# Optimization experiments

Hardware: AMD Instinct MI355X
Metric: run time of the kernel (lower is better)

Reference implementation:

```python
import jax, jax.numpy as jnp
import numpy as np

D, NP, NC, ITERS = 2048, 64, 32, 3
B, L = 4, 4096
EPS = 1e-6


def setup_inputs() -> dict:
    key = jax.random.key(0)
    ks = jax.random.split(key, 10)
    sc = lambda k, shape, s: (jax.random.normal(k, shape, jnp.float32) * s)
    return {
        "x": jax.random.normal(ks[0], (B, L, D), jnp.float32),
        "prop_w": sc(ks[1], (NP, D), 0.02),
        "prop_b": jnp.zeros((NP,), jnp.float32),
        "constraint_mat": sc(ks[2], (NC, NP), 0.1),
        "polarity": sc(ks[3], (NC, NP), 0.1),
        "corr_w1": sc(ks[4], (2 * NP, 2 * NP), 0.08),
        "corr_b1": jnp.zeros((2 * NP,), jnp.float32),
        "corr_w2": sc(ks[5], (NP, 2 * NP), 0.08),
        "corr_b2": jnp.zeros((NP,), jnp.float32),
        "cons_w": sc(ks[6], (1, NC), 0.1),
        "cons_b": jnp.zeros((1,), jnp.float32),
        "emb_w": sc(ks[7], (D, NP), 0.02),
        "emb_b": jnp.zeros((D,), jnp.float32),
        "norm_w": jnp.ones((D,), jnp.float32),
    }


def reference(x, prop_w, prop_b, constraint_mat, polarity,
              corr_w1, corr_b1, corr_w2, corr_b2,
              cons_w, cons_b, emb_w, emb_b, norm_w):
    n_p = prop_w.shape[0]
    n_c = constraint_mat.shape[0]
    W = jax.nn.sigmoid(constraint_mat)  # [n_c, n_p] constraint strength
    P = jax.nn.sigmoid(polarity)        # [n_c, n_p] polarity

    def check(props):
        # mean_j(W_ij*p_j + P_ij*(1-p_j)) == (p @ W.T + (1-p) @ P.T) / n_p
        return (props @ W.T + (1.0 - props) @ P.T) / n_p  # [B,L,n_c]

    props = jax.nn.sigmoid(x @ prop_w.T + prop_b)  # [B,L,n_p]
    for _ in range(ITERS):
        violation = 1.0 - check(props)                 # [B,L,n_c]
        viol_signal = (violation @ W) / (n_c + 1e-06)  # [B,L,n_p]
        h = jnp.concatenate([props, viol_signal], axis=-1)  # [B,L,2*n_p]
        h = jax.nn.gelu(h @ corr_w1.T + corr_b1, approximate=False)
        props = jax.nn.sigmoid(h @ corr_w2.T + corr_b2)

    satisfaction = check(props)                              # [B,L,n_c]
    consistency = jax.nn.sigmoid(satisfaction @ cons_w.T + cons_b)  # [B,L,1]
    violation_loss = jnp.mean(1.0 - satisfaction)
    symbolic = props @ emb_w.T + emb_b                       # [B,L,D]
    y = x + symbolic * consistency
    y = y * jax.lax.rsqrt(jnp.mean(y * y, axis=-1, keepdims=True) + EPS) * norm_w
    return (y, props, satisfaction, consistency, violation_loss)
```

## Files before the change

kernel.cpp:

```cpp
#include <hip/hip_runtime.h>
#include <hip/hip_bf16.h>
#include <cstdint>

#define D     2048
#define NP    64
#define NC    32
#define T     16384

#define Y_OFF   0
#define P_OFF   33554432
#define S_OFF   34603008
#define C_OFF   35127296
#define L_OFF   35143680

#define WS_LPART 0
#define WS_SUMP  1024
#define WS_PWF   1056
#define WS_EF    66592
#define WS_W1F   132128
#define WS_W2F   140320
#define WS_WMF   144416
#define WS_WLF   145440

typedef short short8 __attribute__((ext_vector_type(8)));
typedef float f32x4 __attribute__((ext_vector_type(4)));

__device__ __forceinline__ float sigf(float z) { return 1.0f / (1.0f + __expf(-z)); }
__device__ __forceinline__ short f2bf(float f) {
  unsigned u = __float_as_uint(f);
  return (short)((u + 0x8000u) >> 16);
}
__device__ __forceinline__ unsigned pk2(float a, float b) {
  return ((unsigned)(unsigned short)f2bf(a)) | (((unsigned)(unsigned short)f2bf(b)) << 16);
}

__global__ __launch_bounds__(256) void k0_prep(const float* __restrict__ cm, const float* __restrict__ pol,
                                               const float* __restrict__ w1, const float* __restrict__ w2,
                                               const float* __restrict__ pw, const float* __restrict__ ew,
                                               float* __restrict__ ws) {
  int gid = blockIdx.x * 256 + threadIdx.x;
  int stride = gridDim.x * 256;
  short* pwF = (short*)(ws + WS_PWF);
  for (int idx = gid; idx < 64 * 4 * 64; idx += stride) {
    int kc = idx >> 8, jt = (idx >> 6) & 3, l = idx & 63;
    int j = 16 * jt + (l & 15), k = 32 * kc + 8 * (l >> 4);
    const float* src = &pw[(size_t)j * D + k];
    short8 v;
#pragma unroll
    for (int e = 0; e < 8; ++e) v[e] = f2bf(src[e]);
    *(short8*)&pwF[idx * 8] = v;
  }
  short* eF = (short*)(ws + WS_EF);
  for (int idx = gid; idx < 128 * 2 * 64; idx += stride) {
    int dt = idx >> 7, kc = (idx >> 6) & 1, l = idx & 63;
    int d = 16 * dt + (l & 15), j = 32 * kc + 8 * (l >> 4);
    const float* src = &ew[(size_t)d * NP + j];
    short8 v;
#pragma unroll
    for (int e = 0; e < 8; ++e) v[e] = f2bf(src[e]);
    *(short8*)&eF[idx * 8] = v;
  }
  short* w1F = (short*)(ws + WS_W1F);
  for (int idx = gid; idx < 8 * 4 * 64; idx += stride) {
    int nt = idx >> 8, kc = (idx >> 6) & 3, l = idx & 63;
    int m = 16 * nt + (l & 15), k = 32 * kc + 8 * (l >> 4);
    const float* src = &w1[(size_t)m * 128 + k];
    short8 v;
#pragma unroll
    for (int e = 0; e < 8; ++e) v[e] = f2bf(src[e]);
    *(short8*)&w1F[idx * 8] = v;
  }
  short* w2F = (short*)(ws + WS_W2F);
  for (int idx = gid; idx < 4 * 4 * 64; idx += stride) {
    int nt = idx >> 8, kc = (idx >> 6) & 3, l = idx & 63;
    int j = 16 * nt + (l & 15), k = 32 * kc + 8 * (l >> 4);
    const float* src = &w2[(size_t)j * 128 + k];
    short8 v;
#pragma unroll
    for (int e = 0; e < 8; ++e) v[e] = f2bf(src[e]);
    *(short8*)&w2F[idx * 8] = v;
  }
  short* wmF = (short*)(ws + WS_WMF);
  for (int idx = gid; idx < 2 * 2 * 64; idx += stride) {
    int nt = idx >> 7, kc = (idx >> 6) & 1, l = idx & 63;
    int i = 16 * nt + (l & 15), j = 32 * kc + 8 * (l >> 4);
    short8 v;
#pragma unroll
    for (int e = 0; e < 8; ++e)
      v[e] = f2bf(sigf(cm[i * 64 + j + e]) - sigf(pol[i * 64 + j + e]));
    *(short8*)&wmF[idx * 8] = v;
  }
  short* wlF = (short*)(ws + WS_WLF);
  for (int idx = gid; idx < 4 * 64; idx += stride) {
    int nt = idx >> 6, l = idx & 63;
    int j = 16 * nt + (l & 15), i0 = 8 * (l >> 4);
    short8 v;
#pragma unroll
    for (int e = 0; e < 8; ++e) v[e] = f2bf(sigf(cm[(i0 + e) * 64 + j]));
    *(short8*)&wlF[idx * 8] = v;
  }
  if (gid < NC) {
    float s = 0.f;
    for (int j = 0; j < NP; ++j) s += sigf(pol[gid * NP + j]);
    ws[WS_SUMP + gid] = s;
  }
}

__global__ __launch_bounds__(256) void k1_props(const float* __restrict__ x, const float* __restrict__ ws,
                                                const float* __restrict__ pb, float* __restrict__ props0) {
  __shared__ char XT[8192];
  int tid = threadIdx.x, lane = tid & 63;
  int jt = __builtin_amdgcn_readfirstlane(tid >> 6);
  int wv = tid >> 6;
  int t0 = blockIdx.x * 16;
  int lr = lane & 15, lg = lane >> 4;
  int c64 = tid & 63;
  const short* pwF = (const short*)(ws + WS_PWF);

  f32x4 acc = {0.f, 0.f, 0.f, 0.f};
  for (int c = 0; c < 8; ++c) {
    float4 st[4];
#pragma unroll
    for (int j = 0; j < 4; ++j)
      st[j] = *(const float4*)&x[(size_t)(t0 + wv + 4 * j) * D + 256 * c + 4 * c64];
    __syncthreads();
#pragma unroll
    for (int j = 0; j < 4; ++j) {
      int tt = wv + 4 * j;
      int off = (tt * 512 + 8 * c64) ^ ((tt & 7) << 4);
      *(uint2*)(XT + off) = make_uint2(pk2(st[j].x, st[j].y), pk2(st[j].z, st[j].w));
    }
    __syncthreads();
#pragma unroll
    for (int kcL = 0; kcL < 8; ++kcL) {
      const short8 b = *(const short8*)(XT + ((lr * 512 + 64 * kcL + 16 * lg) ^ ((lr & 7) << 4)));
      const short8 a = *(const short8*)&pwF[(((8 * c + kcL) * 4 + jt) * 64 + lane) * 8];
      acc = __builtin_amdgcn_mfma_f32_16x16x32_bf16(a, b, acc, 0, 0, 0);
    }
  }
  int j0 = 16 * jt + 4 * lg;
  const float4 pbv = *(const float4*)&pb[j0];
  float4 o;
  o.x = sigf(acc[0] + pbv.x); o.y = sigf(acc[1] + pbv.y);
  o.z = sigf(acc[2] + pbv.z); o.w = sigf(acc[3] + pbv.w);
  *(float4*)&props0[(size_t)(t0 + lr) * 64 + j0] = o;
}

__global__ __launch_bounds__(64) void k2_iter(const float* __restrict__ ws,
                                              const float* __restrict__ b1, const float* __restrict__ b2,
                                              const float* __restrict__ cw, const float* __restrict__ cb,
                                              const float* __restrict__ props0, float* __restrict__ out,
                                              float* __restrict__ lpart) {
  __shared__ char Lraw[9216];
  char* Hb = Lraw;
  char* H2b = Lraw + 4096;
  char* SBb = Lraw + 8192;
  int lane = threadIdx.x & 63;
  int lr = lane & 15, lg = lane >> 4;
  int t0 = blockIdx.x * 16;
  const short8* w1F = (const short8*)(ws + WS_W1F);
  const short8* w2F = (const short8*)(ws + WS_W2F);
  const short8* wmF = (const short8*)(ws + WS_WMF);
  const short8* wlF = (const short8*)(ws + WS_WLF);
  const float* SUMP = ws + WS_SUMP;

  float b1v[8], b2v[4], sumpv[2], cwv[2];
#pragma unroll
  for (int nt = 0; nt < 8; ++nt) b1v[nt] = b1[16 * nt + lr];
#pragma unroll
  for (int nt = 0; nt < 4; ++nt) b2v[nt] = b2[16 * nt + lr];
#pragma unroll
  for (int nt = 0; nt < 2; ++nt) { sumpv[nt] = SUMP[16 * nt + lr]; cwv[nt] = cw[16 * nt + lr]; }
  float cb0 = cb[0];

#pragma unroll
  for (int r = 0; r < 4; ++r) {
    int idx = r * 64 + lane;
    int t = idx >> 4, c4 = idx & 15;
    const float4 v = *(const float4*)&props0[(size_t)(t0 + t) * 64 + 4 * c4];
    int off = (t * 256 + c4 * 8) ^ ((t & 7) << 4);
    *(unsigned*)(Hb + off) = pk2(v.x, v.y);
    *(unsigned*)(Hb + off + 4) = pk2(v.z, v.w);
  }
  __syncthreads();

  const f32x4 zf = {0.f, 0.f, 0.f, 0.f};
  f32x4 s0, s1;

#define LDF(base, row, kelem, rowB) \
  (*(const short8*)((base) + ((((row) * (rowB)) + (kelem) * 2) ^ (((row) & 7) << 4))))
#define STBF(base, row, kelem, rowB, val) \
  (*(short*)((base) + ((((row) * (rowB)) + (kelem) * 2) ^ (((row) & 7) << 4))) = f2bf(val))

  for (int it = 0; it < 3; ++it) {
    short8 ap0 = LDF(Hb, lr, 8 * lg, 256);
    short8 ap1 = LDF(Hb, lr, 32 + 8 * lg, 256);
    s0 = zf; s1 = zf;
    s0 = __builtin_amdgcn_mfma_f32_16x16x32_bf16(ap0, wmF[0 * 64 + lane], s0, 0, 0, 0);
    s0 = __builtin_amdgcn_mfma_f32_16x16x32_bf16(ap1, wmF[1 * 64 + lane], s0, 0, 0, 0);
    s1 = __builtin_amdgcn_mfma_f32_16x16x32_bf16(ap0, wmF[2 * 64 + lane], s1, 0, 0, 0);
    s1 = __builtin_amdgcn_mfma_f32_16x16x32_bf16(ap1, wmF[3 * 64 + lane], s1, 0, 0, 0);
#pragma unroll
    for (int q = 0; q < 4; ++q) {
      int t = 4 * lg + q;
      STBF(SBb, t, lr, 64, 1.f - (s0[q] + sumpv[0]) * (1.f / 64.f));
      STBF(SBb, t, 16 + lr, 64, 1.f - (s1[q] + sumpv[1]) * (1.f / 64.f));
    }
    __syncthreads();

    short8 as = LDF(SBb, lr, 8 * lg, 64);
    f32x4 vv0 = __builtin_amdgcn_mfma_f32_16x16x32_bf16(as, wlF[0 * 64 + lane], zf, 0, 0, 0);
    f32x4 vv1 = __builtin_amdgcn_mfma_f32_16x16x32_bf16(as, wlF[1 * 64 + lane], zf, 0, 0, 0);
    f32x4 vv2 = __builtin_amdgcn_mfma_f32_16x16x32_bf16(as, wlF[2 * 64 + lane], zf, 0, 0, 0);
    f32x4 vv3 = __builtin_amdgcn_mfma_f32_16x16x32_bf16(as, wlF[3 * 64 + lane], zf, 0, 0, 0);
    const float vs = 1.0f / (32.0f + 1e-6f);
#pragma unroll
    for (int q = 0; q < 4; ++q) {
      int t = 4 * lg + q;
      STBF(Hb, t, 64 + lr, 256, vv0[q] * vs);
      STBF(Hb, t, 64 + 16 + lr, 256, vv1[q] * vs);
      STBF(Hb, t, 64 + 32 + lr, 256, vv2[q] * vs);
      STBF(Hb, t, 64 + 48 + lr, 256, vv3[q] * vs);
    }
    __syncthreads();

    short8 ah2 = LDF(Hb, lr, 64 + 8 * lg, 256);
    short8 ah3 = LDF(Hb, lr, 96 + 8 * lg, 256);
    f32x4 g1[8];
#pragma unroll
    for (int nt = 0; nt < 8; ++nt) {
      f32x4 a = zf;
      a = __builtin_amdgcn_mfma_f32_16x16x32_bf16(ap0, w1F[(nt * 4 + 0) * 64 + lane], a, 0, 0, 0);
      a = __builtin_amdgcn_mfma_f32_16x16x32_bf16(ap1, w1F[(nt * 4 + 1) * 64 + lane], a, 0, 0, 0);
      a = __builtin_amdgcn_mfma_f32_16x16x32_bf16(ah2, w1F[(nt * 4 + 2) * 64 + lane], a, 0, 0, 0);
      a = __builtin_amdgcn_mfma_f32_16x16x32_bf16(ah3, w1F[(nt * 4 + 3) * 64 + lane], a, 0, 0, 0);
      g1[nt] = a;
    }
#pragma unroll
    for (int nt = 0; nt < 8; ++nt) {
#pragma unroll
      for (int q = 0; q < 4; ++q) {
        float v = g1[nt][q] + b1v[nt];
        float gl = 0.5f * v * (1.0f + erff(v * 0.70710678118654752f));
        STBF(H2b, 4 * lg + q, 16 * nt + lr, 256, gl);
      }
    }
    __syncthreads();

    short8 ab0 = LDF(H2b, lr, 8 * lg, 256);
    short8 ab1 = LDF(H2b, lr, 32 + 8 * lg, 256);
    short8 ab2 = LDF(H2b, lr, 64 + 8 * lg, 256);
    short8 ab3 = LDF(H2b, lr, 96 + 8 * lg, 256);
#pragma unroll
    for (int nt = 0; nt < 4; ++nt) {
      f32x4 a = zf;
      a = __builtin_amdgcn_mfma_f32_16x16x32_bf16(ab0, w2F[(nt * 4 + 0) * 64 + lane], a, 0, 0, 0);
      a = __builtin_amdgcn_mfma_f32_16x16x32_bf16(ab1, w2F[(nt * 4 + 1) * 64 + lane], a, 0, 0, 0);
      a = __builtin_amdgcn_mfma_f32_16x16x32_bf16(ab2, w2F[(nt * 4 + 2) * 64 + lane], a, 0, 0, 0);
      a = __builtin_amdgcn_mfma_f32_16x16x32_bf16(ab3, w2F[(nt * 4 + 3) * 64 + lane], a, 0, 0, 0);
#pragma unroll
      for (int q = 0; q < 4; ++q) {
        int t = 4 * lg + q;
        float p = sigf(a[q] + b2v[nt]);
        STBF(Hb, t, 16 * nt + lr, 256, p);
        if (it == 2) out[P_OFF + (size_t)(t0 + t) * 64 + 16 * nt + lr] = p;
      }
    }
    __syncthreads();
  }

  {
    short8 ap0 = LDF(Hb, lr, 8 * lg, 256);
    short8 ap1 = LDF(Hb, lr, 32 + 8 * lg, 256);
    s0 = zf; s1 = zf;
    s0 = __builtin_amdgcn_mfma_f32_16x16x32_bf16(ap0, wmF[0 * 64 + lane], s0, 0, 0, 0);
    s0 = __builtin_amdgcn_mfma_f32_16x16x32_bf16(ap1, wmF[1 * 64 + lane], s0, 0, 0, 0);
    s1 = __builtin_amdgcn_mfma_f32_16x16x32_bf16(ap0, wmF[2 * 64 + lane], s1, 0, 0, 0);
    s1 = __builtin_amdgcn_mfma_f32_16x16x32_bf16(ap1, wmF[3 * 64 + lane], s1, 0, 0, 0);
    float ls = 0.f;
    float csum[4];
#pragma unroll
    for (int q = 0; q < 4; ++q) {
      int t = 4 * lg + q;
      float sa = (s0[q] + sumpv[0]) * (1.f / 64.f);
      float sb = (s1[q] + sumpv[1]) * (1.f / 64.f);
      out[S_OFF + (size_t)(t0 + t) * 32 + lr] = sa;
      out[S_OFF + (size_t)(t0 + t) * 32 + 16 + lr] = sb;
      ls += (1.f - sa) + (1.f - sb);
      csum[q] = cwv[0] * sa + cwv[1] * sb;
    }
#pragma unroll
    for (int m = 1; m <= 8; m <<= 1) {
#pragma unroll
      for (int q = 0; q < 4; ++q) csum[q] += __shfl_xor(csum[q], m);
    }
    if (lr == 0) {
#pragma unroll
      for (int q = 0; q < 4; ++q)
        out[C_OFF + t0 + 4 * lg + q] = sigf(csum[q] + cb0);
    }
#pragma unroll
    for (int m = 1; m <= 32; m <<= 1) ls += __shfl_xor(ls, m);
    if (lane == 0) lpart[blockIdx.x] = ls;
  }
#undef LDF
#undef STBF
}

__global__ __launch_bounds__(512, 4) void k3n(const float* __restrict__ x, const float* __restrict__ ws,
                                              const float* __restrict__ eb, const float* __restrict__ nw,
                                              const float* __restrict__ lpart, float* __restrict__ out) {
  __shared__ float ssp[8][16];
  __shared__ float sc16[16];
  int tid = threadIdx.x, lane = tid & 63;
  int wu = __builtin_amdgcn_readfirstlane(tid >> 6);
  int t0 = blockIdx.x * 16;
  int lr = lane & 15, lg = lane >> 4;
  const short* eF = (const short*)(ws + WS_EF);

  if (blockIdx.x == 0 && wu == 7) {
    float v = 0.f;
#pragma unroll
    for (int r = 0; r < 16; ++r) v += lpart[lane + 64 * r];
#pragma unroll
    for (int m = 1; m <= 32; m <<= 1) v += __shfl_xor(v, m);
    if (lane == 0) out[L_OFF] = v * (1.0f / (16384.0f * 32.0f));
  }

  const float* pr = out + P_OFF + (size_t)(t0 + lr) * 64 + 8 * lg;
  const float4 q0 = *(const float4*)pr;
  const float4 q1 = *(const float4*)(pr + 4);
  const float4 q2 = *(const float4*)(pr + 32);
  const float4 q3 = *(const float4*)(pr + 36);
  short8 p0, p1;
  p0[0] = f2bf(q0.x); p0[1] = f2bf(q0.y); p0[2] = f2bf(q0.z); p0[3] = f2bf(q0.w);
  p0[4] = f2bf(q1.x); p0[5] = f2bf(q1.y); p0[6] = f2bf(q1.z); p0[7] = f2bf(q1.w);
  p1[0] = f2bf(q2.x); p1[1] = f2bf(q2.y); p1[2] = f2bf(q2.z); p1[3] = f2bf(q2.w);
  p1[4] = f2bf(q3.x); p1[5] = f2bf(q3.y); p1[6] = f2bf(q3.z); p1[7] = f2bf(q3.w);

  float consv = out[C_OFF + t0 + lr];

  uint2 yv[16];
  float ss = 0.f;
#pragma unroll
  for (int dt2 = 0; dt2 < 16; ++dt2) {
    int dt = wu * 16 + dt2;
    const short8 e0 = *(const short8*)&eF[((dt * 2 + 0) * 64 + lane) * 8];
    const short8 e1 = *(const short8*)&eF[((dt * 2 + 1) * 64 + lane) * 8];
    f32x4 acc = {0.f, 0.f, 0.f, 0.f};
    acc = __builtin_amdgcn_mfma_f32_16x16x32_bf16(e0, p0, acc, 0, 0, 0);
    acc = __builtin_amdgcn_mfma_f32_16x16x32_bf16(e1, p1, acc, 0, 0, 0);
    int d0 = 16 * dt + 4 * lg;
    const float4 ebv = *(const float4*)&eb[d0];
    const float4 xv = *(const float4*)&x[(size_t)(t0 + lr) * D + d0];
    float y0 = fmaf(acc[0] + ebv.x, consv, xv.x);
    float y1 = fmaf(acc[1] + ebv.y, consv, xv.y);
    float y2 = fmaf(acc[2] + ebv.z, consv, xv.z);
    float y3 = fmaf(acc[3] + ebv.w, consv, xv.w);
    ss += y0 * y0 + y1 * y1 + y2 * y2 + y3 * y3;
    yv[dt2] = make_uint2(pk2(y0, y1), pk2(y2, y3));
  }
  ss += __shfl_xor(ss, 16);
  ss += __shfl_xor(ss, 32);
  if (lg == 0) ssp[wu][lr] = ss;
  __syncthreads();
  if (tid < 16) {
    float s = 0.f;
#pragma unroll
    for (int w = 0; w < 8; ++w) s += ssp[w][tid];
    sc16[tid] = rsqrtf(s * (1.0f / 2048.0f) + 1e-6f);
  }
  __syncthreads();
  float sc = sc16[lr];
#pragma unroll
  for (int dt2 = 0; dt2 < 16; ++dt2) {
    int d0 = 16 * (wu * 16 + dt2) + 4 * lg;
    const float4 nwv = *(const float4*)&nw[d0];
    uint2 p = yv[dt2];
    float4 o;
    o.x = __uint_as_float(p.x << 16) * sc * nwv.x;
    o.y = __uint_as_float(p.x & 0xffff0000u) * sc * nwv.y;
    o.z = __uint_as_float(p.y << 16) * sc * nwv.z;
    o.w = __uint_as_float(p.y & 0xffff0000u) * sc * nwv.w;
    *(float4*)&out[Y_OFF + (size_t)(t0 + lr) * D + d0] = o;
  }
}

extern "C" void kernel_launch(void* const* d_in, const int* in_sizes, int n_in,
                              void* d_out, int out_size, void* d_ws, size_t ws_size,
                              hipStream_t stream) {
  (void)in_sizes; (void)n_in; (void)out_size; (void)ws_size;
  const float* x   = (const float*)d_in[0];
  const float* pw  = (const float*)d_in[1];
  const float* pb  = (const float*)d_in[2];
  const float* cm  = (const float*)d_in[3];
  const float* pol = (const float*)d_in[4];
  const float* w1  = (const float*)d_in[5];
  const float* b1  = (const float*)d_in[6];
  const float* w2  = (const float*)d_in[7];
  const float* b2  = (const float*)d_in[8];
  const float* cw  = (const float*)d_in[9];
  const float* cb  = (const float*)d_in[10];
  const float* ew  = (const float*)d_in[11];
  const float* eb  = (const float*)d_in[12];
  const float* nw  = (const float*)d_in[13];
  float* out = (float*)d_out;
  float* ws  = (float*)d_ws;

  hipLaunchKernelGGL(k0_prep, dim3(128), dim3(256), 0, stream, cm, pol, w1, w2, pw, ew, ws);
  hipLaunchKernelGGL(k1_props, dim3(1024), dim3(256), 0, stream, x, ws, pb, out + Y_OFF);
  hipLaunchKernelGGL(k2_iter, dim3(1024), dim3(64), 0, stream, ws, b1, b2, cw, cb,
                     out + Y_OFF, out, ws + WS_LPART);
  hipLaunchKernelGGL(k3n, dim3(1024), dim3(512), 0, stream, x, ws, eb, nw,
                     ws + WS_LPART, out);
}
```

Baseline: 125.6 us.

## Fuse iterative correction kernel into embedding/RMSNorm kernel with single-wave prologue

Merges the per-token iteration kernel (k2) into the final embedding+norm kernel, so wave 0 of each 512-thread block runs the three correction iterations and the satisfaction/consistency step. Props and consistency then pass through LDS instead of global memory. The other waves prefetch their x rows into registers while wave 0 works, and wave 0 uses LDS waitcnt fences in place of block barriers. Initial props go to workspace instead of the y buffer, and the loss reduction moves to a tiny separate kernel. The trade-off is that seven waves idle during the serial iteration phase and the 16 float4 prefetch registers raise register pressure.

```diff
diff --git a/kernel.cpp b/kernel.cpp
--- a/kernel.cpp
+++ b/kernel.cpp
@@ -21,6 +21,7 @@
 #define WS_W2F   140320
 #define WS_WMF   144416
 #define WS_WLF   145440
+#define WS_PROPS0 146464
 
 typedef short short8 __attribute__((ext_vector_type(8)));
 typedef float f32x4 __attribute__((ext_vector_type(4)));
@@ -146,199 +147,189 @@
   *(float4*)&props0[(size_t)(t0 + lr) * 64 + j0] = o;
 }
 
-__global__ __launch_bounds__(64) void k2_iter(const float* __restrict__ ws,
+__global__ __launch_bounds__(512, 4) void k3f(const float* __restrict__ x, const float* __restrict__ ws,
                                               const float* __restrict__ b1, const float* __restrict__ b2,
                                               const float* __restrict__ cw, const float* __restrict__ cb,
-                                              const float* __restrict__ props0, float* __restrict__ out,
-                                              float* __restrict__ lpart) {
-  __shared__ char Lraw[9216];
+                                              const float* __restrict__ eb, const float* __restrict__ nw,
+                                              const float* __restrict__ props0,
+                                              float* __restrict__ out, float* __restrict__ lpart) {
+  __shared__ __align__(16) char Lraw[9216];
+  __shared__ float cons16[16];
+  __shared__ float ssp[8][16];
+  __shared__ float sc16[16];
   char* Hb = Lraw;
   char* H2b = Lraw + 4096;
   char* SBb = Lraw + 8192;
-  int lane = threadIdx.x & 63;
-  int lr = lane & 15, lg = lane >> 4;
-  int t0 = blockIdx.x * 16;
-  const short8* w1F = (const short8*)(ws + WS_W1F);
-  const short8* w2F = (const short8*)(ws + WS_W2F);
-  const short8* wmF = (const short8*)(ws + WS_WMF);
-  const short8* wlF = (const short8*)(ws + WS_WLF);
-  const float* SUMP = ws + WS_SUMP;
-
-  float b1v[8], b2v[4], sumpv[2], cwv[2];
-#pragma unroll
-  for (int nt = 0; nt < 8; ++nt) b1v[nt] = b1[16 * nt + lr];
-#pragma unroll
-  for (int nt = 0; nt < 4; ++nt) b2v[nt] = b2[16 * nt + lr];
-#pragma unroll
-  for (int nt = 0; nt < 2; ++nt) { sumpv[nt] = SUMP[16 * nt + lr]; cwv[nt] = cw[16 * nt + lr]; }
-  float cb0 = cb[0];
-
-#pragma unroll
-  for (int r = 0; r < 4; ++r) {
-    int idx = r * 64 + lane;
-    int t = idx >> 4, c4 = idx & 15;
-    const float4 v = *(const float4*)&props0[(size_t)(t0 + t) * 64 + 4 * c4];
-    int off = (t * 256 + c4 * 8) ^ ((t & 7) << 4);
-    *(unsigned*)(Hb + off) = pk2(v.x, v.y);
-    *(unsigned*)(Hb + off + 4) = pk2(v.z, v.w);
-  }
-  __syncthreads();
-
-  const f32x4 zf = {0.f, 0.f, 0.f, 0.f};
-  f32x4 s0, s1;
-
-#define LDF(base, row, kelem, rowB) \
-  (*(const short8*)((base) + ((((row) * (rowB)) + (kelem) * 2) ^ (((row) & 7) << 4))))
-#define STBF(base, row, kelem, rowB, val) \
-  (*(short*)((base) + ((((row) * (rowB)) + (kelem) * 2) ^ (((row) & 7) << 4))) = f2bf(val))
-
-  for (int it = 0; it < 3; ++it) {
-    short8 ap0 = LDF(Hb, lr, 8 * lg, 256);
-    short8 ap1 = LDF(Hb, lr, 32 + 8 * lg, 256);
-    s0 = zf; s1 = zf;
-    s0 = __builtin_amdgcn_mfma_f32_16x16x32_bf16(ap0, wmF[0 * 64 + lane], s0, 0, 0, 0);
-    s0 = __builtin_amdgcn_mfma_f32_16x16x32_bf16(ap1, wmF[1 * 64 + lane], s0, 0, 0, 0);
-    s1 = __builtin_amdgcn_mfma_f32_16x16x32_bf16(ap0, wmF[2 * 64 + lane], s1, 0, 0, 0);
-    s1 = __builtin_amdgcn_mfma_f32_16x16x32_bf16(ap1, wmF[3 * 64 + lane], s1, 0, 0, 0);
-#pragma unroll
-    for (int q = 0; q < 4; ++q) {
-      int t = 4 * lg + q;
-      STBF(SBb, t, lr, 64, 1.f - (s0[q] + sumpv[0]) * (1.f / 64.f));
-      STBF(SBb, t, 16 + lr, 64, 1.f - (s1[q] + sumpv[1]) * (1.f / 64.f));
-    }
-    __syncthreads();
-
-    short8 as = LDF(SBb, lr, 8 * lg, 64);
-    f32x4 vv0 = __builtin_amdgcn_mfma_f32_16x16x32_bf16(as, wlF[0 * 64 + lane], zf, 0, 0, 0);
-    f32x4 vv1 = __builtin_amdgcn_mfma_f32_16x16x32_bf16(as, wlF[1 * 64 + lane], zf, 0, 0, 0);
-    f32x4 vv2 = __builtin_amdgcn_mfma_f32_16x16x32_bf16(as, wlF[2 * 64 + lane], zf, 0, 0, 0);
-    f32x4 vv3 = __builtin_amdgcn_mfma_f32_16x16x32_bf16(as, wlF[3 * 64 + lane], zf, 0, 0, 0);
-    const float vs = 1.0f / (32.0f + 1e-6f);
-#pragma unroll
-    for (int q = 0; q < 4; ++q) {
-      int t = 4 * lg + q;
-      STBF(Hb, t, 64 + lr, 256, vv0[q] * vs);
-      STBF(Hb, t, 64 + 16 + lr, 256, vv1[q] * vs);
-      STBF(Hb, t, 64 + 32 + lr, 256, vv2[q] * vs);
-      STBF(Hb, t, 64 + 48 + lr, 256, vv3[q] * vs);
-    }
-    __syncthreads();
-
-    short8 ah2 = LDF(Hb, lr, 64 + 8 * lg, 256);
-    short8 ah3 = LDF(Hb, lr, 96 + 8 * lg, 256);
-    f32x4 g1[8];
-#pragma unroll
-    for (int nt = 0; nt < 8; ++nt) {
-      f32x4 a = zf;
-      a = __builtin_amdgcn_mfma_f32_16x16x32_bf16(ap0, w1F[(nt * 4 + 0) * 64 + lane], a, 0, 0, 0);
-      a = __builtin_amdgcn_mfma_f32_16x16x32_bf16(ap1, w1F[(nt * 4 + 1) * 64 + lane], a, 0, 0, 0);
-      a = __builtin_amdgcn_mfma_f32_16x16x32_bf16(ah2, w1F[(nt * 4 + 2) * 64 + lane], a, 0, 0, 0);
-      a = __builtin_amdgcn_mfma_f32_16x16x32_bf16(ah3, w1F[(nt * 4 + 3) * 64 + lane], a, 0, 0, 0);
-      g1[nt] = a;
-    }
-#pragma unroll
-    for (int nt = 0; nt < 8; ++nt) {
-#pragma unroll
-      for (int q = 0; q < 4; ++q) {
-        float v = g1[nt][q] + b1v[nt];
-        float gl = 0.5f * v * (1.0f + erff(v * 0.70710678118654752f));
-        STBF(H2b, 4 * lg + q, 16 * nt + lr, 256, gl);
-      }
-    }
-    __syncthreads();
-
-    short8 ab0 = LDF(H2b, lr, 8 * lg, 256);
-    short8 ab1 = LDF(H2b, lr, 32 + 8 * lg, 256);
-    short8 ab2 = LDF(H2b, lr, 64 + 8 * lg, 256);
-    short8 ab3 = LDF(H2b, lr, 96 + 8 * lg, 256);
-#pragma unroll
-    for (int nt = 0; nt < 4; ++nt) {
-      f32x4 a = zf;
-      a = __builtin_amdgcn_mfma_f32_16x16x32_bf16(ab0, w2F[(nt * 4 + 0) * 64 + lane], a, 0, 0, 0);
-      a = __builtin_amdgcn_mfma_f32_16x16x32_bf16(ab1, w2F[(nt * 4 + 1) * 64 + lane], a, 0, 0, 0);
-      a = __builtin_amdgcn_mfma_f32_16x16x32_bf16(ab2, w2F[(nt * 4 + 2) * 64 + lane], a, 0, 0, 0);
-      a = __builtin_amdgcn_mfma_f32_16x16x32_bf16(ab3, w2F[(nt * 4 + 3) * 64 + lane], a, 0, 0, 0);
-#pragma unroll
-      for (int q = 0; q < 4; ++q) {
-        int t = 4 * lg + q;
-        float p = sigf(a[q] + b2v[nt]);
-        STBF(Hb, t, 16 * nt + lr, 256, p);
-        if (it == 2) out[P_OFF + (size_t)(t0 + t) * 64 + 16 * nt + lr] = p;
-      }
-    }
-    __syncthreads();
-  }
-
-  {
-    short8 ap0 = LDF(Hb, lr, 8 * lg, 256);
-    short8 ap1 = LDF(Hb, lr, 32 + 8 * lg, 256);
-    s0 = zf; s1 = zf;
-    s0 = __builtin_amdgcn_mfma_f32_16x16x32_bf16(ap0, wmF[0 * 64 + lane], s0, 0, 0, 0);
-    s0 = __builtin_amdgcn_mfma_f32_16x16x32_bf16(ap1, wmF[1 * 64 + lane], s0, 0, 0, 0);
-    s1 = __builtin_amdgcn_mfma_f32_16x16x32_bf16(ap0, wmF[2 * 64 + lane], s1, 0, 0, 0);
-    s1 = __builtin_amdgcn_mfma_f32_16x16x32_bf16(ap1, wmF[3 * 64 + lane], s1, 0, 0, 0);
-    float ls = 0.f;
-    float csum[4];
-#pragma unroll
-    for (int q = 0; q < 4; ++q) {
-      int t = 4 * lg + q;
-      float sa = (s0[q] + sumpv[0]) * (1.f / 64.f);
-      float sb = (s1[q] + sumpv[1]) * (1.f / 64.f);
-      out[S_OFF + (size_t)(t0 + t) * 32 + lr] = sa;
-      out[S_OFF + (size_t)(t0 + t) * 32 + 16 + lr] = sb;
-      ls += (1.f - sa) + (1.f - sb);
-      csum[q] = cwv[0] * sa + cwv[1] * sb;
-    }
-#pragma unroll
-    for (int m = 1; m <= 8; m <<= 1) {
-#pragma unroll
-      for (int q = 0; q < 4; ++q) csum[q] += __shfl_xor(csum[q], m);
-    }
-    if (lr == 0) {
-#pragma unroll
-      for (int q = 0; q < 4; ++q)
-        out[C_OFF + t0 + 4 * lg + q] = sigf(csum[q] + cb0);
-    }
-#pragma unroll
-    for (int m = 1; m <= 32; m <<= 1) ls += __shfl_xor(ls, m);
-    if (lane == 0) lpart[blockIdx.x] = ls;
-  }
-#undef LDF
-#undef STBF
-}
-
-__global__ __launch_bounds__(512, 4) void k3n(const float* __restrict__ x, const float* __restrict__ ws,
-                                              const float* __restrict__ eb, const float* __restrict__ nw,
-                                              const float* __restrict__ lpart, float* __restrict__ out) {
-  __shared__ float ssp[8][16];
-  __shared__ float sc16[16];
   int tid = threadIdx.x, lane = tid & 63;
   int wu = __builtin_amdgcn_readfirstlane(tid >> 6);
   int t0 = blockIdx.x * 16;
   int lr = lane & 15, lg = lane >> 4;
   const short* eF = (const short*)(ws + WS_EF);
 
-  if (blockIdx.x == 0 && wu == 7) {
-    float v = 0.f;
-#pragma unroll
-    for (int r = 0; r < 16; ++r) v += lpart[lane + 64 * r];
-#pragma unroll
-    for (int m = 1; m <= 32; m <<= 1) v += __shfl_xor(v, m);
-    if (lane == 0) out[L_OFF] = v * (1.0f / (16384.0f * 32.0f));
-  }
-
-  const float* pr = out + P_OFF + (size_t)(t0 + lr) * 64 + 8 * lg;
-  const float4 q0 = *(const float4*)pr;
-  const float4 q1 = *(const float4*)(pr + 4);
-  const float4 q2 = *(const float4*)(pr + 32);
-  const float4 q3 = *(const float4*)(pr + 36);
-  short8 p0, p1;
-  p0[0] = f2bf(q0.x); p0[1] = f2bf(q0.y); p0[2] = f2bf(q0.z); p0[3] = f2bf(q0.w);
-  p0[4] = f2bf(q1.x); p0[5] = f2bf(q1.y); p0[6] = f2bf(q1.z); p0[7] = f2bf(q1.w);
-  p1[0] = f2bf(q2.x); p1[1] = f2bf(q2.y); p1[2] = f2bf(q2.z); p1[3] = f2bf(q2.w);
-  p1[4] = f2bf(q3.x); p1[5] = f2bf(q3.y); p1[6] = f2bf(q3.z); p1[7] = f2bf(q3.w);
-
-  float consv = out[C_OFF + t0 + lr];
+#define LDSFENCE do { asm volatile("s_waitcnt lgkmcnt(0)" ::: "memory"); \
+                      __builtin_amdgcn_sched_barrier(0); } while (0)
+#define LDF(base, row, kelem, rowB) \
+  (*(const short8*)((base) + ((((row) * (rowB)) + (kelem) * 2) ^ (((row) & 7) << 4))))
+#define STBF(base, row, kelem, rowB, val) \
+  (*(short*)((base) + ((((row) * (rowB)) + (kelem) * 2) ^ (((row) & 7) << 4))) = f2bf(val))
+
+  if (wu == 0) {
+    const short8* w1F = (const short8*)(ws + WS_W1F);
+    const short8* w2F = (const short8*)(ws + WS_W2F);
+    const short8* wmF = (const short8*)(ws + WS_WMF);
+    const short8* wlF = (const short8*)(ws + WS_WLF);
+    const float* SUMP = ws + WS_SUMP;
+
+    float b1v[8], b2v[4], sumpv[2], cwv[2];
+#pragma unroll
+    for (int nt = 0; nt < 8; ++nt) b1v[nt] = b1[16 * nt + lr];
+#pragma unroll
+    for (int nt = 0; nt < 4; ++nt) b2v[nt] = b2[16 * nt + lr];
+#pragma unroll
+    for (int nt = 0; nt < 2; ++nt) { sumpv[nt] = SUMP[16 * nt + lr]; cwv[nt] = cw[16 * nt + lr]; }
+    float cb0 = cb[0];
+
+#pragma unroll
+    for (int r = 0; r < 4; ++r) {
+      int idx = r * 64 + lane;
+      int t = idx >> 4, c4 = idx & 15;
+      const float4 v = *(const float4*)&props0[(size_t)(t0 + t) * 64 + 4 * c4];
+      int off = (t * 256 + c4 * 8) ^ ((t & 7) << 4);
+      *(unsigned*)(Hb + off) = pk2(v.x, v.y);
+      *(unsigned*)(Hb + off + 4) = pk2(v.z, v.w);
+    }
+    LDSFENCE;
+
+    const f32x4 zf = {0.f, 0.f, 0.f, 0.f};
+    f32x4 s0, s1;
+
+    for (int it = 0; it < 3; ++it) {
+      short8 ap0 = LDF(Hb, lr, 8 * lg, 256);
+      short8 ap1 = LDF(Hb, lr, 32 + 8 * lg, 256);
+      s0 = zf; s1 = zf;
+      s0 = __builtin_amdgcn_mfma_f32_16x16x32_bf16(ap0, wmF[0 * 64 + lane], s0, 0, 0, 0);
+      s0 = __builtin_amdgcn_mfma_f32_16x16x32_bf16(ap1, wmF[1 * 64 + lane], s0, 0, 0, 0);
+      s1 = __builtin_amdgcn_mfma_f32_16x16x32_bf16(ap0, wmF[2 * 64 + lane], s1, 0, 0, 0);
+      s1 = __builtin_amdgcn_mfma_f32_16x16x32_bf16(ap1, wmF[3 * 64 + lane], s1, 0, 0, 0);
+#pragma unroll
+      for (int q = 0; q < 4; ++q) {
+        int t = 4 * lg + q;
+        STBF(SBb, t, lr, 64, 1.f - (s0[q] + sumpv[0]) * (1.f / 64.f));
+        STBF(SBb, t, 16 + lr, 64, 1.f - (s1[q] + sumpv[1]) * (1.f / 64.f));
+      }
+      LDSFENCE;
+
+      short8 as = LDF(SBb, lr, 8 * lg, 64);
+      f32x4 vv0 = __builtin_amdgcn_mfma_f32_16x16x32_bf16(as, wlF[0 * 64 + lane], zf, 0, 0, 0);
+      f32x4 vv1 = __builtin_amdgcn_mfma_f32_16x16x32_bf16(as, wlF[1 * 64 + lane], zf, 0, 0, 0);
+      f32x4 vv2 = __builtin_amdgcn_mfma_f32_16x16x32_bf16(as, wlF[2 * 64 + lane], zf, 0, 0, 0);
+      f32x4 vv3 = __builtin_amdgcn_mfma_f32_16x16x32_bf16(as, wlF[3 * 64 + lane], zf, 0, 0, 0);
+      const float vs = 1.0f / (32.0f + 1e-6f);
+#pragma unroll
+      for (int q = 0; q < 4; ++q) {
+        int t = 4 * lg + q;
+        STBF(Hb, t, 64 + lr, 256, vv0[q] * vs);
+        STBF(Hb, t, 64 + 16 + lr, 256, vv1[q] * vs);
+        STBF(Hb, t, 64 + 32 + lr, 256, vv2[q] * vs);
+        STBF(Hb, t, 64 + 48 + lr, 256, vv3[q] * vs);
+      }
+      LDSFENCE;
+
+      short8 ah2 = LDF(Hb, lr, 64 + 8 * lg, 256);
+      short8 ah3 = LDF(Hb, lr, 96 + 8 * lg, 256);
+      f32x4 g1[8];
+#pragma unroll
+      for (int nt = 0; nt < 8; ++nt) {
+        f32x4 a = zf;
+        a = __builtin_amdgcn_mfma_f32_16x16x32_bf16(ap0, w1F[(nt * 4 + 0) * 64 + lane], a, 0, 0, 0);
+        a = __builtin_amdgcn_mfma_f32_16x16x32_bf16(ap1, w1F[(nt * 4 + 1) * 64 + lane], a, 0, 0, 0);
+        a = __builtin_amdgcn_mfma_f32_16x16x32_bf16(ah2, w1F[(nt * 4 + 2) * 64 + lane], a, 0, 0, 0);
+        a = __builtin_amdgcn_mfma_f32_16x16x32_bf16(ah3, w1F[(nt * 4 + 3) * 64 + lane], a, 0, 0, 0);
+        g1[nt] = a;
+      }
+#pragma unroll
+      for (int nt = 0; nt < 8; ++nt) {
+#pragma unroll
+        for (int q = 0; q < 4; ++q) {
+          float v = g1[nt][q] + b1v[nt];
+          float gl = 0.5f * v * (1.0f + erff(v * 0.70710678118654752f));
+          STBF(H2b, 4 * lg + q, 16 * nt + lr, 256, gl);
+        }
+      }
+      LDSFENCE;
+
+      short8 ab0 = LDF(H2b, lr, 8 * lg, 256);
+      short8 ab1 = LDF(H2b, lr, 32 + 8 * lg, 256);
+      short8 ab2 = LDF(H2b, lr, 64 + 8 * lg, 256);
+      short8 ab3 = LDF(H2b, lr, 96 + 8 * lg, 256);
+#pragma unroll
+      for (int nt = 0; nt < 4; ++nt) {
+        f32x4 a = zf;
+        a = __builtin_amdgcn_mfma_f32_16x16x32_bf16(ab0, w2F[(nt * 4 + 0) * 64 + lane], a, 0, 0, 0);
+        a = __builtin_amdgcn_mfma_f32_16x16x32_bf16(ab1, w2F[(nt * 4 + 1) * 64 + lane], a, 0, 0, 0);
+        a = __builtin_amdgcn_mfma_f32_16x16x32_bf16(ab2, w2F[(nt * 4 + 2) * 64 + lane], a, 0, 0, 0);
+        a = __builtin_amdgcn_mfma_f32_16x16x32_bf16(ab3, w2F[(nt * 4 + 3) * 64 + lane], a, 0, 0, 0);
+#pragma unroll
+        for (int q = 0; q < 4; ++q) {
+          int t = 4 * lg + q;
+          float p = sigf(a[q] + b2v[nt]);
+          STBF(Hb, t, 16 * nt + lr, 256, p);
+          if (it == 2) out[P_OFF + (size_t)(t0 + t) * 64 + 16 * nt + lr] = p;
+        }
+      }
+      LDSFENCE;
+    }
+
+    {
+      short8 ap0 = LDF(Hb, lr, 8 * lg, 256);
+      short8 ap1 = LDF(Hb, lr, 32 + 8 * lg, 256);
+      s0 = zf; s1 = zf;
+      s0 = __builtin_amdgcn_mfma_f32_16x16x32_bf16(ap0, wmF[0 * 64 + lane], s0, 0, 0, 0);
+      s0 = __builtin_amdgcn_mfma_f32_16x16x32_bf16(ap1, wmF[1 * 64 + lane], s0, 0, 0, 0);
+      s1 = __builtin_amdgcn_mfma_f32_16x16x32_bf16(ap0, wmF[2 * 64 + lane], s1, 0, 0, 0);
+      s1 = __builtin_amdgcn_mfma_f32_16x16x32_bf16(ap1, wmF[3 * 64 + lane], s1, 0, 0, 0);
+      float ls = 0.f;
+      float csum[4];
+#pragma unroll
+      for (int q = 0; q < 4; ++q) {
+        int t = 4 * lg + q;
+        float sa = (s0[q] + sumpv[0]) * (1.f / 64.f);
+        float sb = (s1[q] + sumpv[1]) * (1.f / 64.f);
+        out[S_OFF + (size_t)(t0 + t) * 32 + lr] = sa;
+        out[S_OFF + (size_t)(t0 + t) * 32 + 16 + lr] = sb;
+        ls += (1.f - sa) + (1.f - sb);
+        csum[q] = cwv[0] * sa + cwv[1] * sb;
+      }
+#pragma unroll
+      for (int m = 1; m <= 8; m <<= 1) {
+#pragma unroll
+        for (int q = 0; q < 4; ++q) csum[q] += __shfl_xor(csum[q], m);
+      }
+      if (lr == 0) {
+#pragma unroll
+        for (int q = 0; q < 4; ++q) {
+          float cv = sigf(csum[q] + cb0);
+          cons16[4 * lg + q] = cv;
+          out[C_OFF + t0 + 4 * lg + q] = cv;
+        }
+      }
+#pragma unroll
+      for (int m = 1; m <= 32; m <<= 1) ls += __shfl_xor(ls, m);
+      if (lane == 0) lpart[blockIdx.x] = ls;
+    }
+  }
+
+  float4 xr[16];
+#pragma unroll
+  for (int dt2 = 0; dt2 < 16; ++dt2) {
+    int d0 = 16 * (wu * 16 + dt2) + 4 * lg;
+    xr[dt2] = *(const float4*)&x[(size_t)(t0 + lr) * D + d0];
+  }
+  __syncthreads();
+
+  short8 p0 = LDF(Hb, lr, 8 * lg, 256);
+  short8 p1 = LDF(Hb, lr, 32 + 8 * lg, 256);
+  float consv = cons16[lr];
 
   uint2 yv[16];
   float ss = 0.f;
@@ -352,11 +343,10 @@
     acc = __builtin_amdgcn_mfma_f32_16x16x32_bf16(e1, p1, acc, 0, 0, 0);
     int d0 = 16 * dt + 4 * lg;
     const float4 ebv = *(const float4*)&eb[d0];
-    const float4 xv = *(const float4*)&x[(size_t)(t0 + lr) * D + d0];
-    float y0 = fmaf(acc[0] + ebv.x, consv, xv.x);
-    float y1 = fmaf(acc[1] + ebv.y, consv, xv.y);
-    float y2 = fmaf(acc[2] + ebv.z, consv, xv.z);
-    float y3 = fmaf(acc[3] + ebv.w, consv, xv.w);
+    float y0 = fmaf(acc[0] + ebv.x, consv, xr[dt2].x);
+    float y1 = fmaf(acc[1] + ebv.y, consv, xr[dt2].y);
+    float y2 = fmaf(acc[2] + ebv.z, consv, xr[dt2].z);
+    float y3 = fmaf(acc[3] + ebv.w, consv, xr[dt2].w);
     ss += y0 * y0 + y1 * y1 + y2 * y2 + y3 * y3;
     yv[dt2] = make_uint2(pk2(y0, y1), pk2(y2, y3));
   }
@@ -384,6 +374,22 @@
     o.w = __uint_as_float(p.y & 0xffff0000u) * sc * nwv.w;
     *(float4*)&out[Y_OFF + (size_t)(t0 + lr) * D + d0] = o;
   }
+#undef LDF
+#undef STBF
+#undef LDSFENCE
+}
+
+__global__ __launch_bounds__(256) void k4_loss(const float* __restrict__ lpart, float* __restrict__ loss) {
+  __shared__ float w[4];
+  int tid = threadIdx.x;
+  float v = 0.f;
+#pragma unroll
+  for (int r = 0; r < 4; ++r) v += lpart[tid + 256 * r];
+  for (int o = 32; o > 0; o >>= 1) v += __shfl_down(v, o);
+  if ((tid & 63) == 0) w[tid >> 6] = v;
+  __syncthreads();
+  if (tid == 0)
+    loss[0] = (w[0] + w[1] + w[2] + w[3]) * (1.0f / (16384.0f * 32.0f));
 }
 
 extern "C" void kernel_launch(void* const* d_in, const int* in_sizes, int n_in,
@@ -408,9 +414,8 @@
   float* ws  = (float*)d_ws;
 
   hipLaunchKernelGGL(k0_prep, dim3(128), dim3(256), 0, stream, cm, pol, w1, w2, pw, ew, ws);
-  hipLaunchKernelGGL(k1_props, dim3(1024), dim3(256), 0, stream, x, ws, pb, out + Y_OFF);
-  hipLaunchKernelGGL(k2_iter, dim3(1024), dim3(64), 0, stream, ws, b1, b2, cw, cb,
-                     out + Y_OFF, out, ws + WS_LPART);
-  hipLaunchKernelGGL(k3n, dim3(1024), dim3(512), 0, stream, x, ws, eb, nw,
-                     ws + WS_LPART, out);
-}
+  hipLaunchKernelGGL(k1_props, dim3(1024), dim3(256), 0, stream, x, ws, pb, ws + WS_PROPS0);
+  hipLaunchKernelGGL(k3f, dim3(1024), dim3(512), 0, stream, x, ws, b1, b2, cw, cb, eb, nw,
+                     ws + WS_PROPS0, out, ws + WS_LPART);
+  hipLaunchKernelGGL(k4_loss, dim3(1), dim3(256), 0, stream, ws + WS_LPART, out + L_OFF);
+}
```

Result: slower. 229.7 us (+82.8%).
